# Optimization experiments

Hardware: AMD Instinct MI355X
Metric: run time of the kernel (lower is better)

## Reference

```python
import jax, jax.numpy as jnp
import numpy as np

EPS = 1e-8

def setup_inputs() -> dict:
    key = jax.random.key(0)
    k1, k2, k3 = jax.random.split(key, 3)
    B, A = 4, 2048
    positions = jax.random.normal(k1, (B, A, 3), dtype=jnp.float32)
    neighbors = jax.random.randint(k2, (B, A, A), 0, A, dtype=jnp.int64)
    neighbor_mask = jax.random.randint(k3, (B, A), 0, 2).astype(bool)
    return {"positions": positions, "neighbors": neighbors, "neighbor_mask": neighbor_mask}

def _safe_norm(dist_vec):
    # torch.norm has zero (sub)gradient at 0; guard sqrt for jax parity
    d2 = jnp.sum(dist_vec * dist_vec, axis=-1)  # [B, A, N]
    safe = jnp.sqrt(jnp.where(d2 > 0, d2, 1.0))
    return jnp.where(d2 > 0, safe, 0.0)

def reference(positions, neighbors, neighbor_mask):
    B, A, _ = positions.shape
    # gather neighbor positions: pos_xyz[b, i, j] = positions[b, neighbors[b, i, j]]
    pos_xyz = positions[jnp.arange(B)[:, None, None], neighbors]  # [B, A, N, 3]
    dist_vec = pos_xyz - positions[:, :, None, :]                  # [B, A, N, 3]
    distances = _safe_norm(dist_vec)                               # [B, A, N]
    distances = 1.0 / (distances + EPS)
    # pairwise mask = outer product of per-atom mask (requires N == A)
    mask2 = neighbor_mask[:, :, None] & neighbor_mask[:, None, :]  # [B, A, A]
    eye = jnp.eye(A, dtype=bool)[None]
    distances = jnp.where(eye, 0.0, distances)   # zero diagonal
    distances = jnp.where(mask2, distances, 0.0)  # mask out invalid pairs
    return distances
```

## Files before the change

### kernel.cpp

```cpp
#include <hip/hip_runtime.h>


typedef float f4 __attribute__((ext_vector_type(4)));

constexpr int A_DIM = 2048;
constexpr int WPB   = 8;
constexpr int NTHR  = WPB * 64;

__global__ __launch_bounds__(NTHR, 8) void atom_distances_kernel(
    const float* __restrict__ pos,
    const int*   __restrict__ nbr,
    const int*   __restrict__ mask,
    float*       __restrict__ out) {
  __shared__ float    sxyz[3 * A_DIM];
  __shared__ unsigned smaskbits[A_DIM / 32];

  const int blocks_per_b = A_DIM / WPB;
  const int b  = blockIdx.x / blocks_per_b;
  const int i0 = (blockIdx.x % blocks_per_b) * WPB;

  const float* posb  = pos  + (size_t)b * A_DIM * 3;
  const int*   maskb = mask + (size_t)b * A_DIM;

  for (int t = threadIdx.x; t < A_DIM; t += NTHR) {
    sxyz[t]             = posb[3 * t + 0];
    sxyz[t + A_DIM]     = posb[3 * t + 1];
    sxyz[t + 2 * A_DIM] = posb[3 * t + 2];
  }
  for (int r = 0; r < A_DIM / NTHR; ++r) {
    const int t = r * NTHR + threadIdx.x;
    const unsigned long long bal = __ballot(maskb[t] != 0);
    if ((threadIdx.x & 63) == 0) {
      const int wbase = t >> 5;
      smaskbits[wbase]     = (unsigned)bal;
      smaskbits[wbase + 1] = (unsigned)(bal >> 32);
    }
  }
  __syncthreads();

  const int w    = threadIdx.x >> 6;
  const int lane = threadIdx.x & 63;
  const int i    = i0 + w;

  float* orow = out + ((size_t)b * A_DIM + i) * A_DIM;
  const unsigned mi = (smaskbits[i >> 5] >> (i & 31)) & 1u;

  if (mi == 0) {
    const f4 z = {0.f, 0.f, 0.f, 0.f};
    #pragma unroll
    for (int c = 0; c < 8; ++c)
      __builtin_nontemporal_store(z, reinterpret_cast<f4*>(orow + (c * 64 + lane) * 4));
    return;
  }

  const float pix = sxyz[i];
  const float piy = sxyz[i + A_DIM];
  const float piz = sxyz[i + 2 * A_DIM];

  const int* nrow = nbr + ((size_t)b * A_DIM + i) * A_DIM;

#define LDN(c) (*reinterpret_cast<const int4*>(nrow + ((c) * 64 + lane) * 4))

#define ELEM(nt_, e_, dst_) { \
    const int t_ = (nt_) & (A_DIM - 1); \
    const float dx_ = sxyz[t_] - pix; \
    const float dy_ = sxyz[t_ + A_DIM] - piy; \
    const float dz_ = sxyz[t_ + 2 * A_DIM] - piz; \
    const float d2_ = dx_ * dx_ + dy_ * dy_ + dz_ * dz_; \
    const float inv_ = d2_ > 0.0f ? __builtin_amdgcn_rsqf(d2_) : 1e8f; \
    dst_ = ((((wbits >> (bit + e_)) & 1u) != 0u) & (i != j0 + e_)) ? inv_ : 0.0f; }

#define PROC(c, n) { \
    const int j0 = ((c) * 64 + lane) * 4; \
    const unsigned wbits = smaskbits[(c) * 8 + (lane >> 3)]; \
    const int bit = (lane & 7) * 4; \
    f4 r; \
    ELEM(n.x, 0, r.x); \
    ELEM(n.y, 1, r.y); \
    ELEM(n.z, 2, r.z); \
    ELEM(n.w, 3, r.w); \
    __builtin_nontemporal_store(r, reinterpret_cast<f4*>(orow + j0)); }

  int4 n0 = LDN(0), n1 = LDN(1), n2 = LDN(2), n3 = LDN(3);
  PROC(0, n0); n0 = LDN(4);
  PROC(1, n1); n1 = LDN(5);
  PROC(2, n2); n2 = LDN(6);
  PROC(3, n3); n3 = LDN(7);
  PROC(4, n0);
  PROC(5, n1);
  PROC(6, n2);
  PROC(7, n3);

#undef PROC
#undef ELEM
#undef LDN
}

extern "C" void kernel_launch(void* const* d_in, const int* in_sizes, int n_in,
                              void* d_out, int out_size, void* d_ws, size_t ws_size,
                              hipStream_t stream) {
  const float* pos  = (const float*)d_in[0];
  const int*   nbr  = (const int*)d_in[1];
  const int*   mask = (const int*)d_in[2];
  float*       out  = (float*)d_out;

  const int B = in_sizes[2] / A_DIM;
  const int grid = B * (A_DIM / WPB);

  atom_distances_kernel<<<grid, NTHR, 0, stream>>>(pos, nbr, mask, out);
}
```

Baseline: 22.54 us.

## Compact active rows into a per-batch list and switch to AoS-ish shared layout

Adds a pre-pass kernel that partitions row indices per batch into active-first and inactive-last order, so each block of the main kernel handles rows of uniform mask state and wave divergence between zero-fill and compute rows drops. Shared positions are split into an x array and a packed yz float2 array to cut LDS loads per gather. Nontemporal stores are replaced with ordinary stores. This adds an extra kernel launch, workspace use, and a dependent global load per row index.

Measured after the change: 27.26 us. 1.21x slower.

```diff
diff --git a/kernel.cpp b/kernel.cpp
--- a/kernel.cpp
+++ b/kernel.cpp
@@ -2,30 +2,63 @@
 
 
 typedef float f4 __attribute__((ext_vector_type(4)));
+typedef float f2 __attribute__((ext_vector_type(2)));
 
 constexpr int A_DIM = 2048;
 constexpr int WPB   = 8;
 constexpr int NTHR  = WPB * 64;
 
+__global__ __launch_bounds__(512) void compact_rows_kernel(
+    const int* __restrict__ mask, int* __restrict__ list) {
+  const int b = blockIdx.x;
+  const int* maskb = mask + (size_t)b * A_DIM;
+  int* listb = list + (size_t)b * A_DIM;
+
+  __shared__ int head, tail;
+  if (threadIdx.x == 0) { head = 0; tail = A_DIM; }
+  __syncthreads();
+
+  const int lane = threadIdx.x & 63;
+  for (int r = 0; r < A_DIM; r += 512) {
+    const int row = r + threadIdx.x;
+    const bool act = maskb[row] != 0;
+    const unsigned long long bal = __ballot(act);
+    const int na = __popcll(bal);
+    int baseA = 0, baseI = 0;
+    if (lane == 0) {
+      baseA = atomicAdd(&head, na);
+      baseI = atomicAdd(&tail, -(64 - na)) - (64 - na);
+    }
+    baseA = __shfl(baseA, 0);
+    baseI = __shfl(baseI, 0);
+    const int pa = __popcll(bal & ((1ull << lane) - 1ull));
+    const int pi = lane - pa;
+    if (act) listb[baseA + pa] = row;
+    else     listb[baseI + pi] = row;
+  }
+}
+
 __global__ __launch_bounds__(NTHR, 8) void atom_distances_kernel(
     const float* __restrict__ pos,
     const int*   __restrict__ nbr,
     const int*   __restrict__ mask,
+    const int*   __restrict__ list,
     float*       __restrict__ out) {
-  __shared__ float    sxyz[3 * A_DIM];
+  __shared__ float    sx[A_DIM];
+  __shared__ f2       syz[A_DIM];
   __shared__ unsigned smaskbits[A_DIM / 32];
 
   const int blocks_per_b = A_DIM / WPB;
-  const int b  = blockIdx.x / blocks_per_b;
-  const int i0 = (blockIdx.x % blocks_per_b) * WPB;
+  const int b = blockIdx.x / blocks_per_b;
+  const int s = blockIdx.x % blocks_per_b;
 
   const float* posb  = pos  + (size_t)b * A_DIM * 3;
   const int*   maskb = mask + (size_t)b * A_DIM;
 
   for (int t = threadIdx.x; t < A_DIM; t += NTHR) {
-    sxyz[t]             = posb[3 * t + 0];
-    sxyz[t + A_DIM]     = posb[3 * t + 1];
-    sxyz[t + 2 * A_DIM] = posb[3 * t + 2];
+    sx[t]  = posb[3 * t + 0];
+    f2 yz; yz.x = posb[3 * t + 1]; yz.y = posb[3 * t + 2];
+    syz[t] = yz;
   }
   for (int r = 0; r < A_DIM / NTHR; ++r) {
     const int t = r * NTHR + threadIdx.x;
@@ -40,7 +73,7 @@
 
   const int w    = threadIdx.x >> 6;
   const int lane = threadIdx.x & 63;
-  const int i    = i0 + w;
+  const int i    = list ? list[(size_t)b * A_DIM + s * WPB + w] : s * WPB + w;
 
   float* orow = out + ((size_t)b * A_DIM + i) * A_DIM;
   const unsigned mi = (smaskbits[i >> 5] >> (i & 31)) & 1u;
@@ -49,13 +82,12 @@
     const f4 z = {0.f, 0.f, 0.f, 0.f};
     #pragma unroll
     for (int c = 0; c < 8; ++c)
-      __builtin_nontemporal_store(z, reinterpret_cast<f4*>(orow + (c * 64 + lane) * 4));
+      *reinterpret_cast<f4*>(orow + (c * 64 + lane) * 4) = z;
     return;
   }
 
-  const float pix = sxyz[i];
-  const float piy = sxyz[i + A_DIM];
-  const float piz = sxyz[i + 2 * A_DIM];
+  const float pix = sx[i];
+  const f2    piyz = syz[i];
 
   const int* nrow = nbr + ((size_t)b * A_DIM + i) * A_DIM;
 
@@ -63,9 +95,11 @@
 
 #define ELEM(nt_, e_, dst_) { \
     const int t_ = (nt_) & (A_DIM - 1); \
-    const float dx_ = sxyz[t_] - pix; \
-    const float dy_ = sxyz[t_ + A_DIM] - piy; \
-    const float dz_ = sxyz[t_ + 2 * A_DIM] - piz; \
+    const float xx_ = sx[t_]; \
+    const f2 yz_ = syz[t_]; \
+    const float dx_ = xx_ - pix; \
+    const float dy_ = yz_.x - piyz.x; \
+    const float dz_ = yz_.y - piyz.y; \
     const float d2_ = dx_ * dx_ + dy_ * dy_ + dz_ * dz_; \
     const float inv_ = d2_ > 0.0f ? __builtin_amdgcn_rsqf(d2_) : 1e8f; \
     dst_ = ((((wbits >> (bit + e_)) & 1u) != 0u) & (i != j0 + e_)) ? inv_ : 0.0f; }
@@ -79,7 +113,7 @@
     ELEM(n.y, 1, r.y); \
     ELEM(n.z, 2, r.z); \
     ELEM(n.w, 3, r.w); \
-    __builtin_nontemporal_store(r, reinterpret_cast<f4*>(orow + j0)); }
+    *reinterpret_cast<f4*>(orow + j0) = r; }
 
   int4 n0 = LDN(0), n1 = LDN(1), n2 = LDN(2), n3 = LDN(3);
   PROC(0, n0); n0 = LDN(4);
@@ -105,7 +139,14 @@
   float*       out  = (float*)d_out;
 
   const int B = in_sizes[2] / A_DIM;
+  const size_t list_bytes = (size_t)B * A_DIM * sizeof(int);
+
+  int* list = nullptr;
+  if (ws_size >= list_bytes) {
+    list = (int*)d_ws;
+    compact_rows_kernel<<<B, 512, 0, stream>>>(mask, list);
+  }
+
   const int grid = B * (A_DIM / WPB);
-
-  atom_distances_kernel<<<grid, NTHR, 0, stream>>>(pos, nbr, mask, out);
+  atom_distances_kernel<<<grid, NTHR, 0, stream>>>(pos, nbr, mask, list, out);
 }
```
